# Performance work log

Hardware: AMD Instinct MI355X
Metric: run time of the kernel (lower is better)

## Reference

```python
import jax, jax.numpy as jnp
import numpy as np

TEMPERATURE = 0.07
EPS = 1e-12  # F.normalize eps


def setup_inputs() -> dict:
    key = jax.random.key(0)
    k1, k2 = jax.random.split(key)
    B, D = 4096, 1024
    return {
        "features_1": jax.random.normal(k1, (B, D), dtype=jnp.float32),
        "features_2": jax.random.normal(k2, (B, D), dtype=jnp.float32),
    }


def _l2_normalize(x):
    n = jnp.sqrt(jnp.sum(x * x, axis=1, keepdims=True))
    return x / jnp.maximum(n, EPS)


def reference(features_1, features_2):
    B = features_1.shape[0]
    f1 = _l2_normalize(features_1)
    f2 = _l2_normalize(features_2)
    f = jnp.concatenate([f1, f2], axis=0)  # [2B, D]
    # cosine sim of already-normalized vectors == plain matmul
    sim = (f @ f.T) / TEMPERATURE  # [2B, 2B]
    # denominator: logsumexp over each row excluding the diagonal (self-sim)
    eye = jnp.eye(2 * B, dtype=bool)
    lse = jax.nn.logsumexp(jnp.where(eye, -jnp.inf, sim), axis=1)  # [2B]
    # positives: cross-view pairs (i+B, i) then (i, i+B)
    idx = jnp.arange(B)
    pos = jnp.concatenate([sim[idx + B, idx], sim[idx, idx + B]], axis=0)  # [2B]
    loss = -jnp.mean(pos - lse)
    return loss
```

## Files before the change

kernel.cpp:

```cpp
#include <hip/hip_runtime.h>
#include <hip/hip_bf16.h>
#include <math.h>

#define INV_T (1.0f / 0.07f)

typedef __bf16 bf16x8 __attribute__((ext_vector_type(8)));
typedef float f32x4 __attribute__((ext_vector_type(4)));

__device__ __forceinline__ void gld16(const void* g, void* l) {
    __builtin_amdgcn_global_load_lds(
        (const __attribute__((address_space(1))) unsigned int*)g,
        (__attribute__((address_space(3))) unsigned int*)l,
        16, 0, 0);
}

__global__ __launch_bounds__(256) void norm_kernel(
    const float4* __restrict__ f1, const float4* __restrict__ f2,
    ushort4* __restrict__ F, float* __restrict__ S, float* __restrict__ P,
    int B) {
    const int i = blockIdx.x;
    const int t = threadIdx.x;

    float4 x = f1[i * 256 + t];
    float4 y = f2[i * 256 + t];

    float s1 = x.x * x.x + x.y * x.y + x.z * x.z + x.w * x.w;
    float s2 = y.x * y.x + y.y * y.y + y.z * y.z + y.w * y.w;
    float dd = x.x * y.x + x.y * y.y + x.z * y.z + x.w * y.w;

    for (int o = 32; o > 0; o >>= 1) {
        s1 += __shfl_down(s1, o);
        s2 += __shfl_down(s2, o);
        dd += __shfl_down(dd, o);
    }
    __shared__ float red[4][3];
    const int wv = t >> 6, ln = t & 63;
    if (ln == 0) { red[wv][0] = s1; red[wv][1] = s2; red[wv][2] = dd; }
    __syncthreads();
    s1 = red[0][0] + red[1][0] + red[2][0] + red[3][0];
    s2 = red[0][1] + red[1][1] + red[2][1] + red[3][1];
    dd = red[0][2] + red[1][2] + red[2][2] + red[3][2];

    const float rn1 = 1.0f / fmaxf(sqrtf(s1), 1e-12f);
    const float rn2 = 1.0f / fmaxf(sqrtf(s2), 1e-12f);

    union { ushort4 u; __hip_bfloat16 h[4]; } p;
    p.h[0] = __float2bfloat16(x.x * rn1);
    p.h[1] = __float2bfloat16(x.y * rn1);
    p.h[2] = __float2bfloat16(x.z * rn1);
    p.h[3] = __float2bfloat16(x.w * rn1);
    F[(size_t)i * 256 + t] = p.u;
    p.h[0] = __float2bfloat16(y.x * rn2);
    p.h[1] = __float2bfloat16(y.y * rn2);
    p.h[2] = __float2bfloat16(y.z * rn2);
    p.h[3] = __float2bfloat16(y.w * rn2);
    F[(size_t)(B + i) * 256 + t] = p.u;

    if (t == 0) {
        P[i] = dd * rn1 * rn2;
        S[i] = 0.0f;
        S[B + i] = 0.0f;
    }
}


#define BARRIER() asm volatile("s_barrier" ::: "memory")
#define VMCNT6()  asm volatile("s_waitcnt vmcnt(6)" ::: "memory")
#define VMCNT0()  asm volatile("s_waitcnt vmcnt(0)" ::: "memory")

#define QUAD_MFMA(MH, NH)                                                     \
    _Pragma("unroll") for (int mi = 0; mi < 4; ++mi)                          \
    _Pragma("unroll") for (int ni = 0; ni < 2; ++ni)                          \
    _Pragma("unroll") for (int ks = 0; ks < 2; ++ks)                          \
        acc[(MH) * 4 + mi][(NH) * 2 + ni] =                                   \
            __builtin_amdgcn_mfma_f32_16x16x32_bf16(                          \
                af[mi][ks], bf[NH][ni][ks],                                   \
                acc[(MH) * 4 + mi][(NH) * 2 + ni], 0, 0, 0);

#define PH_COMPUTE(MH, NH)                                                    \
    BARRIER();                                                                \
    asm volatile("s_waitcnt lgkmcnt(0)" ::: "memory");                        \
    __builtin_amdgcn_sched_barrier(0);                                        \
    __builtin_amdgcn_s_setprio(1);                                            \
    QUAD_MFMA(MH, NH);                                                        \
    __builtin_amdgcn_s_setprio(0);                                            \
    __builtin_amdgcn_sched_barrier(0);

__global__ __launch_bounds__(512, 2) void sim_kernel(
    const ushort* __restrict__ F, float* __restrict__ S, int N) {
    (void)N;
    __shared__ __align__(16) ushort lds[2][2][2][128 * 64];

    const int k = blockIdx.x;
    int tj = (int)((sqrtf(8.0f * (float)k + 1.0f) - 1.0f) * 0.5f);
    while ((tj + 1) * (tj + 2) / 2 <= k) ++tj;
    while (tj * (tj + 1) / 2 > k) --tj;
    const int ti = k - tj * (tj + 1) / 2;
    const int bRow = ti * 256, bCol = tj * 256;

    const int tid = threadIdx.x;
    const int wave = tid >> 6, lane = tid & 63;
    const int wr = wave >> 2, wc = wave & 3;
    const int quad = lane >> 4, l16 = lane & 15;
    const int swz = l16 & 7;

    const int r0 = tid >> 3;
    const int scol = ((tid & 7) ^ (r0 & 7)) * 8;
    const size_t gA = (size_t)(bRow + r0) * 1024 + scol;
    const size_t gB = (size_t)(bCol + r0) * 1024 + scol;

    auto stage = [&](int bsel, int ab, int h, int kb) {
        const ushort* g = F + (ab ? gB : gA) + (size_t)h * (128 * 1024) + kb;
        ushort* l = &lds[bsel][ab][h][tid * 8];
        gld16(g, l);
        gld16(g + 64 * 1024, l + 512 * 8);
    };

    bf16x8 af[4][2];
    bf16x8 bf[2][2][2];
    f32x4 acc[8][4];
#pragma unroll
    for (int a = 0; a < 8; ++a)
#pragma unroll
        for (int b = 0; b < 4; ++b) acc[a][b] = (f32x4){0.0f, 0.0f, 0.0f, 0.0f};

    auto loadA = [&](int bsel, int mh) {
#pragma unroll
        for (int mi = 0; mi < 4; ++mi)
#pragma unroll
            for (int ks = 0; ks < 2; ++ks)
                af[mi][ks] = *(const bf16x8*)&lds[bsel][0][wr]
                    [(mh * 64 + mi * 16 + l16) * 64 + ((ks * 4 + quad) ^ swz) * 8];
    };
    auto loadB = [&](int bsel) {
#pragma unroll
        for (int nh = 0; nh < 2; ++nh)
#pragma unroll
            for (int ni = 0; ni < 2; ++ni)
#pragma unroll
                for (int ks = 0; ks < 2; ++ks)
                    bf[nh][ni][ks] = *(const bf16x8*)&lds[bsel][1][wc >> 1]
                        [((wc & 1) * 64 + nh * 32 + ni * 16 + l16) * 64 +
                         ((ks * 4 + quad) ^ swz) * 8];
    };

    stage(0, 0, 0, 0); stage(0, 0, 1, 0); stage(0, 1, 0, 0); stage(0, 1, 1, 0);
    stage(1, 1, 0, 64); stage(1, 1, 1, 64); stage(1, 0, 0, 64);
    VMCNT6();
    BARRIER();

#pragma unroll 1
    for (int it = 0; it < 7; ++it) {
        const int kb0 = it * 128;
        loadA(0, 0); loadB(0);
        stage(1, 0, 1, kb0 + 64);
        PH_COMPUTE(0, 0);
        BARRIER();
        stage(0, 1, 0, kb0 + 128);
        PH_COMPUTE(0, 1);
        BARRIER();
        loadA(0, 1);
        stage(0, 1, 1, kb0 + 128);
        PH_COMPUTE(1, 0);
        BARRIER();
        stage(0, 0, 0, kb0 + 128);
        PH_COMPUTE(1, 1);
        VMCNT6();
        BARRIER();
        loadA(1, 0); loadB(1);
        stage(0, 0, 1, kb0 + 128);
        PH_COMPUTE(0, 0);
        BARRIER();
        stage(1, 1, 0, kb0 + 192);
        PH_COMPUTE(0, 1);
        BARRIER();
        loadA(1, 1);
        stage(1, 1, 1, kb0 + 192);
        PH_COMPUTE(1, 0);
        BARRIER();
        stage(1, 0, 0, kb0 + 192);
        PH_COMPUTE(1, 1);
        VMCNT6();
        BARRIER();
    }

    loadA(0, 0); loadB(0);
    stage(1, 0, 1, 960);
    QUAD_MFMA(0, 0);
    QUAD_MFMA(0, 1);
    loadA(0, 1);
    QUAD_MFMA(1, 0);
    QUAD_MFMA(1, 1);
    VMCNT0();
    BARRIER();
    loadA(1, 0); loadB(1);
    QUAD_MFMA(0, 0);
    QUAD_MFMA(0, 1);
    loadA(1, 1);
    QUAD_MFMA(1, 0);
    QUAD_MFMA(1, 1);

#pragma unroll
    for (int a = 0; a < 8; ++a)
#pragma unroll
        for (int b = 0; b < 4; ++b)
#pragma unroll
            for (int r = 0; r < 4; ++r) {
                const int gRow = bRow + wr * 128 + (a >> 2) * 64 + (a & 3) * 16 + quad * 4 + r;
                const int gCol = bCol + wc * 64 + (b >> 1) * 32 + (b & 1) * 16 + l16;
                acc[a][b][r] = (gRow < gCol)
                    ? __expf((acc[a][b][r] - 1.0f) * INV_T) : 0.0f;
            }

#pragma unroll
    for (int a = 0; a < 8; ++a)
#pragma unroll
        for (int r = 0; r < 4; ++r) {
            const int gRow = bRow + wr * 128 + (a >> 2) * 64 + (a & 3) * 16 + quad * 4 + r;
            float v = acc[a][0][r] + acc[a][1][r] + acc[a][2][r] + acc[a][3][r];
            v += __shfl_xor(v, 1);
            v += __shfl_xor(v, 2);
            v += __shfl_xor(v, 4);
            v += __shfl_xor(v, 8);
            if (l16 == 0) atomicAdd(&S[gRow], v);
        }

#pragma unroll
    for (int b = 0; b < 4; ++b) {
        float cv = 0.0f;
#pragma unroll
        for (int a = 0; a < 8; ++a)
#pragma unroll
            for (int r = 0; r < 4; ++r) cv += acc[a][b][r];
        cv += __shfl_xor(cv, 16);
        cv += __shfl_xor(cv, 32);
        if (quad == 0) {
            const int gCol = bCol + wc * 64 + (b >> 1) * 32 + (b & 1) * 16 + l16;
            atomicAdd(&S[gCol], cv);
        }
    }
}

__global__ __launch_bounds__(256) void finalize_kernel(
    const float* __restrict__ S, const float* __restrict__ P,
    float* __restrict__ out, int N, int B) {
    float s = 0.0f;
    for (int i = threadIdx.x; i < N; i += 256) s += __logf(S[i]);
    float pp = 0.0f;
    for (int i = threadIdx.x; i < B; i += 256) pp += P[i];
    for (int o = 32; o > 0; o >>= 1) {
        s += __shfl_down(s, o);
        pp += __shfl_down(pp, o);
    }
    __shared__ float red[4][2];
    if ((threadIdx.x & 63) == 0) {
        red[threadIdx.x >> 6][0] = s;
        red[threadIdx.x >> 6][1] = pp;
    }
    __syncthreads();
    if (threadIdx.x == 0) {
        const float sl = red[0][0] + red[1][0] + red[2][0] + red[3][0];
        const float ps = red[0][1] + red[1][1] + red[2][1] + red[3][1];
        out[0] = INV_T + sl / (float)N - ps * (2.0f * INV_T / (float)N);
    }
}

extern "C" void kernel_launch(void* const* d_in, const int* in_sizes, int n_in,
                              void* d_out, int out_size, void* d_ws, size_t ws_size,
                              hipStream_t stream) {
    const int D = 1024;
    const int B = in_sizes[0] / D;
    const int N = 2 * B;
    const int M = N / 256;
    const int ntiles = M * (M + 1) / 2;

    const float* f1 = (const float*)d_in[0];
    const float* f2 = (const float*)d_in[1];

    __hip_bfloat16* F = (__hip_bfloat16*)d_ws;
    float* S = (float*)((char*)d_ws + (size_t)N * D * sizeof(__hip_bfloat16));
    float* P = S + N;

    norm_kernel<<<dim3(B), dim3(256), 0, stream>>>(
        (const float4*)f1, (const float4*)f2, (ushort4*)F, S, P, B);
    sim_kernel<<<dim3(ntiles), dim3(512), 0, stream>>>((const ushort*)F, S, N);
    finalize_kernel<<<dim3(1), dim3(256), 0, stream>>>(S, P, (float*)d_out, N, B);
}
```

Before: 188.9 us.

## Skip below-diagonal MFMA quadrants, reorder tiles, fuse finalize into sim kernel

Diagonal tiles now skip MFMA quadrants that lie entirely below the diagonal, since those results are masked out anyway. Tiles are reordered so off-diagonal tiles come first, spread in an XCD-aware interleave, and diagonal tiles run last. The finalize kernel is removed: the last block to finish, found through an atomic counter, does the logsumexp reduction, which saves one launch. B-fragment LDS loads are split per half and the MFMA loop order is changed to ks-outer. The trade-off is extra branching and a threadfence plus atomic at the end of every block.

```diff
diff --git a/kernel.cpp b/kernel.cpp
--- a/kernel.cpp
+++ b/kernel.cpp
@@ -17,7 +17,7 @@
 __global__ __launch_bounds__(256) void norm_kernel(
     const float4* __restrict__ f1, const float4* __restrict__ f2,
     ushort4* __restrict__ F, float* __restrict__ S, float* __restrict__ P,
-    int B) {
+    int* __restrict__ cnt, int B) {
     const int i = blockIdx.x;
     const int t = threadIdx.x;
 
@@ -60,6 +60,7 @@
         P[i] = dd * rn1 * rn2;
         S[i] = 0.0f;
         S[B + i] = 0.0f;
+        if (i == 0) *cnt = 0;
     }
 }
 
@@ -69,33 +70,43 @@
 #define VMCNT0()  asm volatile("s_waitcnt vmcnt(0)" ::: "memory")
 
 #define QUAD_MFMA(MH, NH)                                                     \
+    _Pragma("unroll") for (int ks = 0; ks < 2; ++ks)                          \
     _Pragma("unroll") for (int mi = 0; mi < 4; ++mi)                          \
     _Pragma("unroll") for (int ni = 0; ni < 2; ++ni)                          \
-    _Pragma("unroll") for (int ks = 0; ks < 2; ++ks)                          \
         acc[(MH) * 4 + mi][(NH) * 2 + ni] =                                   \
             __builtin_amdgcn_mfma_f32_16x16x32_bf16(                          \
                 af[mi][ks], bf[NH][ni][ks],                                   \
                 acc[(MH) * 4 + mi][(NH) * 2 + ni], 0, 0, 0);
 
-#define PH_COMPUTE(MH, NH)                                                    \
+#define PH_COMPUTE(MH, NH, SK)                                                \
     BARRIER();                                                                \
     asm volatile("s_waitcnt lgkmcnt(0)" ::: "memory");                        \
     __builtin_amdgcn_sched_barrier(0);                                        \
-    __builtin_amdgcn_s_setprio(1);                                            \
-    QUAD_MFMA(MH, NH);                                                        \
-    __builtin_amdgcn_s_setprio(0);                                            \
+    if (!(SK)) {                                                              \
+        __builtin_amdgcn_s_setprio(1);                                        \
+        QUAD_MFMA(MH, NH);                                                    \
+        __builtin_amdgcn_s_setprio(0);                                        \
+    }                                                                         \
     __builtin_amdgcn_sched_barrier(0);
 
 __global__ __launch_bounds__(512, 2) void sim_kernel(
-    const ushort* __restrict__ F, float* __restrict__ S, int N) {
-    (void)N;
+    const ushort* __restrict__ F, float* __restrict__ S,
+    const float* __restrict__ P, float* __restrict__ out,
+    int* __restrict__ cnt, int Nn, int Bn, int noff, int chunk) {
     __shared__ __align__(16) ushort lds[2][2][2][128 * 64];
 
-    const int k = blockIdx.x;
-    int tj = (int)((sqrtf(8.0f * (float)k + 1.0f) - 1.0f) * 0.5f);
-    while ((tj + 1) * (tj + 2) / 2 <= k) ++tj;
-    while (tj * (tj + 1) / 2 > k) --tj;
-    const int ti = k - tj * (tj + 1) / 2;
+    const int p = blockIdx.x;
+    int ti, tj;
+    if (p < noff) {
+        const int o = chunk ? (p & 7) * chunk + (p >> 3) : p;
+        int t = (int)((1.0f + sqrtf(8.0f * (float)o + 1.0f)) * 0.5f);
+        while (t * (t - 1) / 2 > o) --t;
+        while ((t + 1) * t / 2 <= o) ++t;
+        tj = t;
+        ti = o - t * (t - 1) / 2;
+    } else {
+        ti = tj = p - noff;
+    }
     const int bRow = ti * 256, bCol = tj * 256;
 
     const int tid = threadIdx.x;
@@ -103,6 +114,12 @@
     const int wr = wave >> 2, wc = wave & 3;
     const int quad = lane >> 4, l16 = lane & 15;
     const int swz = l16 & 7;
+
+    const int rB = bRow + wr * 128, cB = bCol + wc * 64;
+    const bool sk00 = rB > cB + 31;
+    const bool sk01 = rB > cB + 63;
+    const bool sk10 = rB + 64 > cB + 31;
+    const bool sk11 = rB + 64 > cB + 63;
 
     const int r0 = tid >> 3;
     const int scol = ((tid & 7) ^ (r0 & 7)) * 8;
@@ -132,16 +149,14 @@
                 af[mi][ks] = *(const bf16x8*)&lds[bsel][0][wr]
                     [(mh * 64 + mi * 16 + l16) * 64 + ((ks * 4 + quad) ^ swz) * 8];
     };
-    auto loadB = [&](int bsel) {
-#pragma unroll
-        for (int nh = 0; nh < 2; ++nh)
-#pragma unroll
-            for (int ni = 0; ni < 2; ++ni)
-#pragma unroll
-                for (int ks = 0; ks < 2; ++ks)
-                    bf[nh][ni][ks] = *(const bf16x8*)&lds[bsel][1][wc >> 1]
-                        [((wc & 1) * 64 + nh * 32 + ni * 16 + l16) * 64 +
-                         ((ks * 4 + quad) ^ swz) * 8];
+    auto loadB = [&](int bsel, int nh) {
+#pragma unroll
+        for (int ni = 0; ni < 2; ++ni)
+#pragma unroll
+            for (int ks = 0; ks < 2; ++ks)
+                bf[nh][ni][ks] = *(const bf16x8*)&lds[bsel][1][wc >> 1]
+                    [((wc & 1) * 64 + nh * 32 + ni * 16 + l16) * 64 +
+                     ((ks * 4 + quad) ^ swz) * 8];
     };
 
     stage(0, 0, 0, 0); stage(0, 0, 1, 0); stage(0, 1, 0, 0); stage(0, 1, 1, 0);
@@ -152,53 +167,57 @@
 #pragma unroll 1
     for (int it = 0; it < 7; ++it) {
         const int kb0 = it * 128;
-        loadA(0, 0); loadB(0);
+        loadA(0, 0); loadB(0, 0);
         stage(1, 0, 1, kb0 + 64);
-        PH_COMPUTE(0, 0);
-        BARRIER();
+        PH_COMPUTE(0, 0, sk00);
+        BARRIER();
+        loadB(0, 1);
         stage(0, 1, 0, kb0 + 128);
-        PH_COMPUTE(0, 1);
+        PH_COMPUTE(0, 1, sk01);
         BARRIER();
         loadA(0, 1);
         stage(0, 1, 1, kb0 + 128);
-        PH_COMPUTE(1, 0);
+        PH_COMPUTE(1, 0, sk10);
         BARRIER();
         stage(0, 0, 0, kb0 + 128);
-        PH_COMPUTE(1, 1);
+        PH_COMPUTE(1, 1, sk11);
         VMCNT6();
         BARRIER();
-        loadA(1, 0); loadB(1);
+        loadA(1, 0); loadB(1, 0);
         stage(0, 0, 1, kb0 + 128);
-        PH_COMPUTE(0, 0);
-        BARRIER();
+        PH_COMPUTE(0, 0, sk00);
+        BARRIER();
+        loadB(1, 1);
         stage(1, 1, 0, kb0 + 192);
-        PH_COMPUTE(0, 1);
+        PH_COMPUTE(0, 1, sk01);
         BARRIER();
         loadA(1, 1);
         stage(1, 1, 1, kb0 + 192);
-        PH_COMPUTE(1, 0);
+        PH_COMPUTE(1, 0, sk10);
         BARRIER();
         stage(1, 0, 0, kb0 + 192);
-        PH_COMPUTE(1, 1);
+        PH_COMPUTE(1, 1, sk11);
         VMCNT6();
         BARRIER();
     }
 
-    loadA(0, 0); loadB(0);
+    loadA(0, 0); loadB(0, 0);
     stage(1, 0, 1, 960);
-    QUAD_MFMA(0, 0);
-    QUAD_MFMA(0, 1);
+    if (!sk00) { QUAD_MFMA(0, 0); }
+    loadB(0, 1);
+    if (!sk01) { QUAD_MFMA(0, 1); }
     loadA(0, 1);
-    QUAD_MFMA(1, 0);
-    QUAD_MFMA(1, 1);
+    if (!sk10) { QUAD_MFMA(1, 0); }
+    if (!sk11) { QUAD_MFMA(1, 1); }
     VMCNT0();
     BARRIER();
-    loadA(1, 0); loadB(1);
-    QUAD_MFMA(0, 0);
-    QUAD_MFMA(0, 1);
+    loadA(1, 0); loadB(1, 0);
+    if (!sk00) { QUAD_MFMA(0, 0); }
+    loadB(1, 1);
+    if (!sk01) { QUAD_MFMA(0, 1); }
     loadA(1, 1);
-    QUAD_MFMA(1, 0);
-    QUAD_MFMA(1, 1);
+    if (!sk10) { QUAD_MFMA(1, 0); }
+    if (!sk11) { QUAD_MFMA(1, 1); }
 
 #pragma unroll
     for (int a = 0; a < 8; ++a)
@@ -239,29 +258,29 @@
             atomicAdd(&S[gCol], cv);
         }
     }
-}
-
-__global__ __launch_bounds__(256) void finalize_kernel(
-    const float* __restrict__ S, const float* __restrict__ P,
-    float* __restrict__ out, int N, int B) {
+
+    __threadfence();
+    __shared__ int lastFlag;
+    if (tid == 0) lastFlag = (atomicAdd(cnt, 1) == (int)gridDim.x - 1);
+    __syncthreads();
+    if (!lastFlag) return;
+
     float s = 0.0f;
-    for (int i = threadIdx.x; i < N; i += 256) s += __logf(S[i]);
+    for (int i = tid; i < Nn; i += 512) s += __logf(atomicAdd(&S[i], 0.0f));
     float pp = 0.0f;
-    for (int i = threadIdx.x; i < B; i += 256) pp += P[i];
+    for (int i = tid; i < Bn; i += 512) pp += P[i];
     for (int o = 32; o > 0; o >>= 1) {
         s += __shfl_down(s, o);
         pp += __shfl_down(pp, o);
     }
-    __shared__ float red[4][2];
-    if ((threadIdx.x & 63) == 0) {
-        red[threadIdx.x >> 6][0] = s;
-        red[threadIdx.x >> 6][1] = pp;
-    }
+    __shared__ float red[8][2];
+    if (lane == 0) { red[wave][0] = s; red[wave][1] = pp; }
     __syncthreads();
-    if (threadIdx.x == 0) {
-        const float sl = red[0][0] + red[1][0] + red[2][0] + red[3][0];
-        const float ps = red[0][1] + red[1][1] + red[2][1] + red[3][1];
-        out[0] = INV_T + sl / (float)N - ps * (2.0f * INV_T / (float)N);
+    if (tid == 0) {
+        float sl = 0.0f, ps = 0.0f;
+#pragma unroll
+        for (int w = 0; w < 8; ++w) { sl += red[w][0]; ps += red[w][1]; }
+        out[0] = INV_T + sl / (float)Nn - ps * (2.0f * INV_T / (float)Nn);
     }
 }
 
@@ -272,7 +291,9 @@
     const int B = in_sizes[0] / D;
     const int N = 2 * B;
     const int M = N / 256;
-    const int ntiles = M * (M + 1) / 2;
+    const int noff = M * (M - 1) / 2;
+    const int ntiles = noff + M;
+    const int chunk = (noff % 8 == 0) ? noff / 8 : 0;
 
     const float* f1 = (const float*)d_in[0];
     const float* f2 = (const float*)d_in[1];
@@ -280,9 +301,10 @@
     __hip_bfloat16* F = (__hip_bfloat16*)d_ws;
     float* S = (float*)((char*)d_ws + (size_t)N * D * sizeof(__hip_bfloat16));
     float* P = S + N;
+    int* cnt = (int*)(P + B);
 
     norm_kernel<<<dim3(B), dim3(256), 0, stream>>>(
-        (const float4*)f1, (const float4*)f2, (ushort4*)F, S, P, B);
-    sim_kernel<<<dim3(ntiles), dim3(512), 0, stream>>>((const ushort*)F, S, N);
-    finalize_kernel<<<dim3(1), dim3(256), 0, stream>>>(S, P, (float*)d_out, N, B);
+        (const float4*)f1, (const float4*)f2, (ushort4*)F, S, P, cnt, B);
+    sim_kernel<<<dim3(ntiles), dim3(512), 0, stream>>>(
+        (const ushort*)F, S, P, (float*)d_out, cnt, N, B, noff, chunk);
 }
```

Measured after the change: 239.5 us. 26.8% more time.
